# Kernel tuning notes

Measured on AMD Instinct MI355X. Metric: run time of the kernel, lower is better.

## Reference

```python
import jax, jax.numpy as jnp
import numpy as np

DIM, HEADS, HD, WS, SHIFT = 768, 48, 16, 3, 1
EPS = 1e-5


def setup_inputs() -> dict:
    key = jax.random.key(0)
    ks = jax.random.split(key, 6)
    s = 0.02  # init scale for weights
    return {
        "x": jax.random.normal(ks[0], (8, 4096, DIM), jnp.float32),
        "g1": jnp.ones((DIM,), jnp.float32),
        "b1": jnp.zeros((DIM,), jnp.float32),
        "w_qkv": jax.random.normal(ks[1], (DIM, 3 * DIM), jnp.float32) * s,
        "w_proj": jax.random.normal(ks[2], (DIM, DIM), jnp.float32) * s,
        "g2": jnp.ones((DIM,), jnp.float32),
        "b2": jnp.zeros((DIM,), jnp.float32),
        "w_mlp1": jax.random.normal(ks[3], (DIM, 2 * DIM), jnp.float32) * s,
        "b_mlp1": jnp.zeros((2 * DIM,), jnp.float32),
        "w_mlp2": jax.random.normal(ks[4], (2 * DIM, DIM), jnp.float32) * s,
        "b_mlp2": jnp.zeros((DIM,), jnp.float32),
    }


def _ln(x, g, b):
    m = x.mean(-1, keepdims=True)
    v = ((x - m) ** 2).mean(-1, keepdims=True)
    return (x - m) * jax.lax.rsqrt(v + EPS) * g + b


def _shifted_window_attention(x, w_qkv, w_proj):
    B, T, C = x.shape
    pad_r = (WS - T % WS) % WS
    xp = jnp.pad(x, ((0, 0), (0, pad_r), (0, 0)))
    Tp = T + pad_r
    xs = jnp.roll(xp, -SHIFT, axis=1) if SHIFT > 0 else xp
    xw = xs.reshape(B, Tp // WS, WS, C)            # [B, nW, ws, C]
    qkv = (xw @ w_qkv).reshape(B, Tp // WS, WS, 3, HEADS, HD)
    q, k, v = jnp.moveaxis(qkv, 3, 0)              # each [B, nW, ws, H, hd]
    attn = jnp.einsum("bnihd,bnjhd->bnhij", q, k) * (HD ** -0.5)
    attn = jax.nn.softmax(attn, axis=-1)           # [B, nW, H, ws, ws]
    o = jnp.einsum("bnhij,bnjhd->bnihd", attn, v).reshape(B, Tp, C)
    o = o @ w_proj
    if SHIFT > 0:
        o = jnp.roll(o, SHIFT, axis=1)
    return o[:, :T]


def reference(x, g1, b1, w_qkv, w_proj, g2, b2, w_mlp1, b_mlp1, w_mlp2, b_mlp2):
    x = x + _shifted_window_attention(_ln(x, g1, b1), w_qkv, w_proj)
    h = _ln(x, g2, b2)
    x = x + (jax.nn.relu(h @ w_mlp1 + b_mlp1) @ w_mlp2 + b_mlp2)
    return x
```

## Files before the change

### kernel.cpp

```cpp
#include <hip/hip_runtime.h>

#define BATCH 8
#define TLEN  4096
#define DIM   768
#define TP    4098
#define NWIN  1366
#define HEADS 48
#define HD    16
#define MREAL (BATCH*TP)
#define MP    32896
#define M2    (BATCH*TLEN)

typedef unsigned short u16;
typedef __bf16  bf16x8  __attribute__((ext_vector_type(8)));
typedef short   short8v __attribute__((ext_vector_type(8)));
typedef float   float4v __attribute__((ext_vector_type(4)));
typedef u16     u16x4   __attribute__((ext_vector_type(4)));

static __device__ __forceinline__ float bf2f(u16 u) {
  unsigned int x = ((unsigned int)u) << 16;
  return __builtin_bit_cast(float, x);
}
static __device__ __forceinline__ u16 f2bf(float f) {
  unsigned int x = __builtin_bit_cast(unsigned int, f);
  x += 0x7fffu + ((x >> 16) & 1u);
  return (u16)(x >> 16);
}

static __device__ __forceinline__ float4v mfma_bf16(short8v a, short8v b, float4v c) {
  return __builtin_amdgcn_mfma_f32_16x16x32_bf16(
      __builtin_bit_cast(bf16x8, a), __builtin_bit_cast(bf16x8, b), c, 0, 0, 0);
}

static __device__ __forceinline__ void gload_lds16(const u16* src, u16* ldsdst) {
  __builtin_amdgcn_global_load_lds(
      (const __attribute__((address_space(1))) void*)src,
      (__attribute__((address_space(3))) void*)ldsdst,
      16, 0, 0);
}

__global__ __launch_bounds__(256) void cvt_transpose(const float* __restrict__ w,
                                                     u16* __restrict__ wt,
                                                     int K, int N) {
  int idx = blockIdx.x * 256 + threadIdx.x;
  if (idx >= K * N) return;
  int k = idx / N, n = idx - k * N;
  wt[(size_t)n * K + k] = f2bf(w[idx]);
}

template<bool ROLL>
__global__ __launch_bounds__(256) void ln_kernel(const float* __restrict__ x,
                                                 const float* __restrict__ g,
                                                 const float* __restrict__ bet,
                                                 u16* __restrict__ out) {
  int wave = threadIdx.x >> 6, lane = threadIdx.x & 63;
  int row = blockIdx.x * 4 + wave;
  u16* orow = out + (size_t)row * DIM;

  const float* src;
  if (ROLL) {
    bool zero = (row >= MREAL);
    int t = 0, b = 0;
    if (!zero) {
      b = row / TP;
      int m = row - b * TP;
      t = m + 1; if (t == TP) t = 0;
      if (t >= TLEN) zero = true;
    }
    if (zero) {
      u16x4 z = {};
#pragma unroll
      for (int c = 0; c < 3; ++c) *(u16x4*)&orow[c * 256 + lane * 4] = z;
      return;
    }
    src = x + ((size_t)b * TLEN + t) * DIM;
  } else {
    src = x + (size_t)row * DIM;
  }

  float v[12];
  float s = 0.f, s2 = 0.f;
#pragma unroll
  for (int c = 0; c < 3; ++c) {
    float4v f = *(const float4v*)&src[c * 256 + lane * 4];
#pragma unroll
    for (int q = 0; q < 4; ++q) { v[c * 4 + q] = f[q]; s += f[q]; s2 += f[q] * f[q]; }
  }
#pragma unroll
  for (int off = 1; off < 64; off <<= 1) {
    s  += __shfl_xor(s, off);
    s2 += __shfl_xor(s2, off);
  }
  float mean = s * (1.f / DIM);
  float var  = s2 * (1.f / DIM) - mean * mean;
  float rs   = rsqrtf(var + 1e-5f);
#pragma unroll
  for (int c = 0; c < 3; ++c) {
    int col = c * 256 + lane * 4;
    float4v gv = *(const float4v*)&g[col];
    float4v bv = *(const float4v*)&bet[col];
    u16x4 o4;
#pragma unroll
    for (int q = 0; q < 4; ++q) o4[q] = f2bf((v[c * 4 + q] - mean) * rs * gv[q] + bv[q]);
    *(u16x4*)&orow[col] = o4;
  }
}

__global__ __launch_bounds__(256) void lnb_kernel(const u16* __restrict__ xin,
                                                  const float* __restrict__ g,
                                                  const float* __restrict__ bet,
                                                  u16* __restrict__ out) {
  int wave = threadIdx.x >> 6, lane = threadIdx.x & 63;
  int row = blockIdx.x * 4 + wave;
  const u16* src = xin + (size_t)row * DIM;
  u16* orow = out + (size_t)row * DIM;

  float v[12];
  float s = 0.f, s2 = 0.f;
#pragma unroll
  for (int c = 0; c < 3; ++c) {
    u16x4 h = *(const u16x4*)&src[c * 256 + lane * 4];
#pragma unroll
    for (int q = 0; q < 4; ++q) {
      float f = bf2f(h[q]);
      v[c * 4 + q] = f; s += f; s2 += f * f;
    }
  }
#pragma unroll
  for (int off = 1; off < 64; off <<= 1) {
    s  += __shfl_xor(s, off);
    s2 += __shfl_xor(s2, off);
  }
  float mean = s * (1.f / DIM);
  float var  = s2 * (1.f / DIM) - mean * mean;
  float rs   = rsqrtf(var + 1e-5f);
#pragma unroll
  for (int c = 0; c < 3; ++c) {
    int col = c * 256 + lane * 4;
    float4v gv = *(const float4v*)&g[col];
    float4v bv = *(const float4v*)&bet[col];
    u16x4 o4;
#pragma unroll
    for (int q = 0; q < 4; ++q) o4[q] = f2bf((v[c * 4 + q] - mean) * rs * gv[q] + bv[q]);
    *(u16x4*)&orow[col] = o4;
  }
}

__global__ __launch_bounds__(256) void attn_kernel(const u16* __restrict__ qkv,
                                                   u16* __restrict__ o) {
  int gid = blockIdx.x * 256 + threadIdx.x;
  int h = gid % HEADS;
  int w = gid / HEADS;
  int b = w / NWIN, wl = w - b * NWIN;
  size_t row0 = (size_t)b * TP + (size_t)wl * 3;

  float q[3][HD], k[3][HD];
#pragma unroll
  for (int t = 0; t < 3; ++t) {
    const u16* rp = qkv + (row0 + t) * (3 * DIM) + h * HD;
    short8v q0 = *(const short8v*)(rp);
    short8v q1 = *(const short8v*)(rp + 8);
    short8v k0 = *(const short8v*)(rp + DIM);
    short8v k1 = *(const short8v*)(rp + DIM + 8);
#pragma unroll
    for (int d = 0; d < 8; ++d) {
      q[t][d] = bf2f((u16)q0[d]); q[t][d + 8] = bf2f((u16)q1[d]);
      k[t][d] = bf2f((u16)k0[d]); k[t][d + 8] = bf2f((u16)k1[d]);
    }
  }
  float p[3][3];
#pragma unroll
  for (int i = 0; i < 3; ++i)
#pragma unroll
    for (int j = 0; j < 3; ++j) {
      float s = 0.f;
#pragma unroll
      for (int d = 0; d < HD; ++d) s += q[i][d] * k[j][d];
      p[i][j] = s * 0.25f;
    }
#pragma unroll
  for (int i = 0; i < 3; ++i) {
    float mx = fmaxf(p[i][0], fmaxf(p[i][1], p[i][2]));
    float e0 = __expf(p[i][0] - mx), e1 = __expf(p[i][1] - mx), e2 = __expf(p[i][2] - mx);
    float inv = 1.f / (e0 + e1 + e2);
    p[i][0] = e0 * inv; p[i][1] = e1 * inv; p[i][2] = e2 * inv;
  }
  float acc[3][HD];
#pragma unroll
  for (int i = 0; i < 3; ++i)
#pragma unroll
    for (int d = 0; d < HD; ++d) acc[i][d] = 0.f;
#pragma unroll
  for (int t = 0; t < 3; ++t) {
    const u16* rp = qkv + (row0 + t) * (3 * DIM) + 2 * DIM + h * HD;
    short8v v0 = *(const short8v*)(rp);
    short8v v1 = *(const short8v*)(rp + 8);
#pragma unroll
    for (int d = 0; d < 8; ++d) {
      float a = bf2f((u16)v0[d]), bb = bf2f((u16)v1[d]);
#pragma unroll
      for (int i = 0; i < 3; ++i) { acc[i][d] += p[i][t] * a; acc[i][d + 8] += p[i][t] * bb; }
    }
  }
#pragma unroll
  for (int i = 0; i < 3; ++i) {
    u16 tmp[HD];
#pragma unroll
    for (int d = 0; d < HD; ++d) tmp[d] = f2bf(acc[i][d]);
    u16* op = o + (row0 + i) * DIM + h * HD;
    *(short8v*)op = *(short8v*)tmp;
    *(short8v*)(op + 8) = *(short8v*)(tmp + 8);
  }
}

template<int EPI>
__global__ __launch_bounds__(512, 4) void gemm8w(const u16* __restrict__ A,
                                                 const u16* __restrict__ Bt,
                                                 int N, int K,
                                                 u16* __restrict__ outb,
                                                 float* __restrict__ outf,
                                                 const float* __restrict__ residf,
                                                 const u16* __restrict__ residb,
                                                 const float* __restrict__ bias) {
  __shared__ u16 As[2][128 * 32];
  __shared__ u16 Bs[2][128 * 32];
  const int tid = threadIdx.x;
  const int wave = tid >> 6, lane = tid & 63;
  const int wm = wave >> 2, wn = wave & 3;
  const int r = lane & 15, gq = lane >> 4;

  const int nwg = gridDim.x, gx = N >> 7;
  int wg = blockIdx.x;
  int qd = nwg >> 3, rr = nwg & 7, xcd = wg & 7, lid = wg >> 3;
  int swz = (xcd < rr ? xcd * (qd + 1) : rr * (qd + 1) + (xcd - rr) * qd) + lid;
  const int tm = swz / gx, tn = swz - tm * gx;
  const int arow0 = tm * 128, brow0 = tn * 128;

  const int srowS = tid >> 2;
  const int scolS = ((((tid & 3) << 4) ^ (((srowS >> 1) & 3) << 4)) >> 1);

  const int kxS = (((gq << 4) ^ (((r >> 1) & 3) << 4)) >> 1);
  const int rA = wm * 64 + r, rB = wn * 32 + r;

  float4v acc[4][2];
#pragma unroll
  for (int i = 0; i < 4; ++i)
#pragma unroll
    for (int j = 0; j < 2; ++j) acc[i][j] = (float4v){0.f, 0.f, 0.f, 0.f};

  auto stage = [&](int buf, int tk) {
    gload_lds16(A  + (size_t)(arow0 + srowS) * K + tk * 32 + scolS,
                &As[buf][0] + tid * 8);
    gload_lds16(Bt + (size_t)(brow0 + srowS) * K + tk * 32 + scolS,
                &Bs[buf][0] + tid * 8);
  };

  const int NT = K >> 5;
  stage(0, 0);
  for (int t = 0; t < NT; ++t) {
    const int cur = t & 1;
    if (t + 1 < NT) {
      stage(cur ^ 1, t + 1);
      asm volatile("s_waitcnt vmcnt(2)" ::: "memory");
    } else {
      asm volatile("s_waitcnt vmcnt(0)" ::: "memory");
    }
    __builtin_amdgcn_sched_barrier(0);
    __builtin_amdgcn_s_barrier();
    __builtin_amdgcn_sched_barrier(0);

    short8v af[4], bfr[2];
#pragma unroll
    for (int i = 0; i < 4; ++i)
      af[i] = *(const short8v*)&As[cur][(rA + i * 16) * 32 + kxS];
#pragma unroll
    for (int j = 0; j < 2; ++j)
      bfr[j] = *(const short8v*)&Bs[cur][(rB + j * 16) * 32 + kxS];

    __builtin_amdgcn_s_setprio(1);
#pragma unroll
    for (int i = 0; i < 4; ++i)
#pragma unroll
      for (int j = 0; j < 2; ++j)
        acc[i][j] = mfma_bf16(af[i], bfr[j], acc[i][j]);
    __builtin_amdgcn_s_setprio(0);

    asm volatile("s_waitcnt lgkmcnt(0)" ::: "memory");
    __builtin_amdgcn_sched_barrier(0);
    __builtin_amdgcn_s_barrier();
    __builtin_amdgcn_sched_barrier(0);
  }

#pragma unroll
  for (int i = 0; i < 4; ++i) {
#pragma unroll
    for (int j = 0; j < 2; ++j) {
      int colg = brow0 + wn * 32 + j * 16 + r;
      int rowb = arow0 + wm * 64 + i * 16 + gq * 4;
#pragma unroll
      for (int v = 0; v < 4; ++v) {
        int rg = rowb + v;
        float val = acc[i][j][v];
        if constexpr (EPI == 0) {
          outb[(size_t)rg * N + colg] = f2bf(val);
        } else if constexpr (EPI == 1) {
          if (rg < MREAL) {
            int b = rg / TP, m = rg - b * TP;
            int t = m + 1; if (t == TP) t = 0;
            if (t < TLEN) {
              size_t idx = ((size_t)b * TLEN + t) * DIM + colg;
              outb[idx] = f2bf(residf[idx] + val);
            }
          }
        } else if constexpr (EPI == 2) {
          float z = val + bias[colg];
          outb[(size_t)rg * N + colg] = f2bf(z > 0.f ? z : 0.f);
        } else {
          size_t idx = (size_t)rg * N + colg;
          outf[idx] = bf2f(residb[idx]) + val + bias[colg];
        }
      }
    }
  }
}

extern "C" void kernel_launch(void* const* d_in, const int* in_sizes, int n_in,
                              void* d_out, int out_size, void* d_ws, size_t ws_size,
                              hipStream_t stream) {
  const float* x      = (const float*)d_in[0];
  const float* g1     = (const float*)d_in[1];
  const float* b1     = (const float*)d_in[2];
  const float* w_qkv  = (const float*)d_in[3];
  const float* w_proj = (const float*)d_in[4];
  const float* g2     = (const float*)d_in[5];
  const float* b2     = (const float*)d_in[6];
  const float* w_mlp1 = (const float*)d_in[7];
  const float* b_mlp1 = (const float*)d_in[8];
  const float* w_mlp2 = (const float*)d_in[9];
  const float* b_mlp2 = (const float*)d_in[10];
  float* out = (float*)d_out;

  u16* xs     = (u16*)d_ws;
  u16* qkv    = xs     + (size_t)MP * DIM;
  u16* obuf   = qkv    + (size_t)MP * 3 * DIM;
  u16* wqkvT  = obuf   + (size_t)MP * DIM;
  u16* wprojT = wqkvT  + (size_t)3 * DIM * DIM;
  u16* wm1T   = wprojT + (size_t)DIM * DIM;
  u16* wm2T   = wm1T   + (size_t)2 * DIM * DIM;
  u16* resf = xs;
  u16* ln2o = obuf;
  u16* h1   = qkv;

  cvt_transpose<<<(DIM * 3 * DIM + 255) / 256, 256, 0, stream>>>(w_qkv,  wqkvT,  DIM,     3 * DIM);
  cvt_transpose<<<(DIM * DIM + 255)     / 256, 256, 0, stream>>>(w_proj, wprojT, DIM,     DIM);
  cvt_transpose<<<(DIM * 2 * DIM + 255) / 256, 256, 0, stream>>>(w_mlp1, wm1T,   DIM,     2 * DIM);
  cvt_transpose<<<(2 * DIM * DIM + 255) / 256, 256, 0, stream>>>(w_mlp2, wm2T,   2 * DIM, DIM);

  ln_kernel<true><<<MP / 4, 256, 0, stream>>>(x, g1, b1, xs);

  gemm8w<0><<<(MP / 128) * (3 * DIM / 128), 512, 0, stream>>>(
      xs, wqkvT, 3 * DIM, DIM, qkv, nullptr, nullptr, nullptr, nullptr);

  attn_kernel<<<(BATCH * NWIN * HEADS) / 256, 256, 0, stream>>>(qkv, obuf);

  gemm8w<1><<<(MP / 128) * (DIM / 128), 512, 0, stream>>>(
      obuf, wprojT, DIM, DIM, resf, nullptr, x, nullptr, nullptr);

  lnb_kernel<<<M2 / 4, 256, 0, stream>>>(resf, g2, b2, ln2o);

  gemm8w<2><<<(M2 / 128) * (2 * DIM / 128), 512, 0, stream>>>(
      ln2o, wm1T, 2 * DIM, DIM, h1, nullptr, nullptr, nullptr, b_mlp1);

  gemm8w<3><<<(M2 / 128) * (DIM / 128), 512, 0, stream>>>(
      h1, wm2T, DIM, 2 * DIM, nullptr, out, nullptr, resf, b_mlp2);
}
```

Before: 601.1 us.

## Triple-buffer GEMM LDS pipeline with one barrier, fuse weight conversions

The GEMM k-loop moves from double to triple LDS buffering. It now uses a single barrier per iteration and issues the prefetch for tile t+2 after that barrier, so global loads overlap two MFMA steps instead of one. Occupancy in launch_bounds is raised from 4 to 6 to match. The four weight convert-transpose launches are merged into one kernel to cut launch overhead. The cost is more LDS per block (48KB), which may limit how many blocks fit per CU.

```diff
diff --git a/kernel.cpp b/kernel.cpp
--- a/kernel.cpp
+++ b/kernel.cpp
@@ -39,13 +39,27 @@
       16, 0, 0);
 }
 
-__global__ __launch_bounds__(256) void cvt_transpose(const float* __restrict__ w,
-                                                     u16* __restrict__ wt,
-                                                     int K, int N) {
+#define CVT_E0 1769472
+#define CVT_E1 (CVT_E0 + 589824)
+#define CVT_E2 (CVT_E1 + 1179648)
+#define CVT_E3 (CVT_E2 + 1179648)
+__global__ __launch_bounds__(256) void cvt_all(const float* __restrict__ w0,
+                                               const float* __restrict__ w1,
+                                               const float* __restrict__ w2,
+                                               const float* __restrict__ w3,
+                                               u16* __restrict__ t0,
+                                               u16* __restrict__ t1,
+                                               u16* __restrict__ t2,
+                                               u16* __restrict__ t3) {
   int idx = blockIdx.x * 256 + threadIdx.x;
-  if (idx >= K * N) return;
-  int k = idx / N, n = idx - k * N;
-  wt[(size_t)n * K + k] = f2bf(w[idx]);
+  const float* w; u16* wt; int K, N, e;
+  if (idx < CVT_E0)      { w = w0; wt = t0; K = 768;  N = 2304; e = idx; }
+  else if (idx < CVT_E1) { w = w1; wt = t1; K = 768;  N = 768;  e = idx - CVT_E0; }
+  else if (idx < CVT_E2) { w = w2; wt = t2; K = 768;  N = 1536; e = idx - CVT_E1; }
+  else if (idx < CVT_E3) { w = w3; wt = t3; K = 1536; N = 768;  e = idx - CVT_E2; }
+  else return;
+  int k = e / N, n = e - k * N;
+  wt[(size_t)n * K + k] = f2bf(w[e]);
 }
 
 template<bool ROLL>
@@ -214,7 +228,7 @@
 }
 
 template<int EPI>
-__global__ __launch_bounds__(512, 4) void gemm8w(const u16* __restrict__ A,
+__global__ __launch_bounds__(512, 6) void gemm8w(const u16* __restrict__ A,
                                                  const u16* __restrict__ Bt,
                                                  int N, int K,
                                                  u16* __restrict__ outb,
@@ -222,8 +236,8 @@
                                                  const float* __restrict__ residf,
                                                  const u16* __restrict__ residb,
                                                  const float* __restrict__ bias) {
-  __shared__ u16 As[2][128 * 32];
-  __shared__ u16 Bs[2][128 * 32];
+  __shared__ u16 As[3][128 * 32];
+  __shared__ u16 Bs[3][128 * 32];
   const int tid = threadIdx.x;
   const int wave = tid >> 6, lane = tid & 63;
   const int wm = wave >> 2, wn = wave & 3;
@@ -257,38 +271,39 @@
 
   const int NT = K >> 5;
   stage(0, 0);
+  if (NT > 1) stage(1, 1);
+
+  int buf = 0;
   for (int t = 0; t < NT; ++t) {
-    const int cur = t & 1;
     if (t + 1 < NT) {
-      stage(cur ^ 1, t + 1);
       asm volatile("s_waitcnt vmcnt(2)" ::: "memory");
     } else {
       asm volatile("s_waitcnt vmcnt(0)" ::: "memory");
     }
-    __builtin_amdgcn_sched_barrier(0);
-    __builtin_amdgcn_s_barrier();
-    __builtin_amdgcn_sched_barrier(0);
-
-    short8v af[4], bfr[2];
-#pragma unroll
-    for (int i = 0; i < 4; ++i)
-      af[i] = *(const short8v*)&As[cur][(rA + i * 16) * 32 + kxS];
-#pragma unroll
-    for (int j = 0; j < 2; ++j)
-      bfr[j] = *(const short8v*)&Bs[cur][(rB + j * 16) * 32 + kxS];
-
-    __builtin_amdgcn_s_setprio(1);
-#pragma unroll
-    for (int i = 0; i < 4; ++i)
-#pragma unroll
-      for (int j = 0; j < 2; ++j)
-        acc[i][j] = mfma_bf16(af[i], bfr[j], acc[i][j]);
-    __builtin_amdgcn_s_setprio(0);
-
     asm volatile("s_waitcnt lgkmcnt(0)" ::: "memory");
     __builtin_amdgcn_sched_barrier(0);
     __builtin_amdgcn_s_barrier();
     __builtin_amdgcn_sched_barrier(0);
+
+    if (t + 2 < NT) stage((t + 2) % 3, t + 2);
+
+    short8v af[4], bfr[2];
+#pragma unroll
+    for (int i = 0; i < 4; ++i)
+      af[i] = *(const short8v*)&As[buf][(rA + i * 16) * 32 + kxS];
+#pragma unroll
+    for (int j = 0; j < 2; ++j)
+      bfr[j] = *(const short8v*)&Bs[buf][(rB + j * 16) * 32 + kxS];
+
+    __builtin_amdgcn_s_setprio(1);
+#pragma unroll
+    for (int i = 0; i < 4; ++i)
+#pragma unroll
+      for (int j = 0; j < 2; ++j)
+        acc[i][j] = mfma_bf16(af[i], bfr[j], acc[i][j]);
+    __builtin_amdgcn_s_setprio(0);
+
+    buf = (buf + 1 == 3) ? 0 : buf + 1;
   }
 
 #pragma unroll
@@ -351,10 +366,8 @@
   u16* ln2o = obuf;
   u16* h1   = qkv;
 
-  cvt_transpose<<<(DIM * 3 * DIM + 255) / 256, 256, 0, stream>>>(w_qkv,  wqkvT,  DIM,     3 * DIM);
-  cvt_transpose<<<(DIM * DIM + 255)     / 256, 256, 0, stream>>>(w_proj, wprojT, DIM,     DIM);
-  cvt_transpose<<<(DIM * 2 * DIM + 255) / 256, 256, 0, stream>>>(w_mlp1, wm1T,   DIM,     2 * DIM);
-  cvt_transpose<<<(2 * DIM * DIM + 255) / 256, 256, 0, stream>>>(w_mlp2, wm2T,   2 * DIM, DIM);
+  cvt_all<<<(CVT_E3 + 255) / 256, 256, 0, stream>>>(
+      w_qkv, w_proj, w_mlp1, w_mlp2, wqkvT, wprojT, wm1T, wm2T);
 
   ln_kernel<true><<<MP / 4, 256, 0, stream>>>(x, g1, b1, xs);
 
```

New measurement: 596.9 us. About the same (-0.7%).
